# Kernel optimization log

Hardware: AMD Instinct MI355X
Metric: run time of the kernel (lower is better)

Reference implementation:

```python
import jax, jax.numpy as jnp
import numpy as np

B1, B2 = 4096, 4096
DF, MF = 1024, 512
H1, H2, H3, H1_ = 2048, 1024, 512, 1024
DO, MO = 1, 1


def _lin(x, W, b):
    return x @ W.T + b


def setup_inputs() -> dict:
    key = jax.random.key(0)
    ks = jax.random.split(key, 22)

    def w(k, o, i):
        return (jax.random.normal(k, (o, i), jnp.float32) / np.sqrt(i)).astype(jnp.float32)

    def bz(k, o):
        return jax.random.normal(k, (o,), jnp.float32) * 0.01

    return {
        'x1': jax.random.normal(ks[0], (B1, DF), jnp.float32),
        'x2': jax.random.normal(ks[1], (B2, MF), jnp.float32),
        'W1_1': w(ks[2], H1, DF),  'b1_1': bz(ks[3], H1),
        'W1_2': w(ks[4], H2, H1),  'b1_2': bz(ks[5], H2),
        'W1_3': w(ks[6], H3, H2),  'b1_3': bz(ks[7], H3),
        'W1_4': w(ks[8], H2, H3),  'b1_4': bz(ks[9], H2),
        'W1_5': w(ks[10], H1, H2), 'b1_5': bz(ks[11], H1),
        'Wp1':  w(ks[12], DO, H1), 'bp1':  bz(ks[13], DO),
        'W2_1': w(ks[14], H1_, MF), 'b2_1': bz(ks[15], H1_),
        'W2_2': w(ks[16], H3, H1_), 'b2_2': bz(ks[17], H3),
        'W2_3': w(ks[18], H1_, H3), 'b2_3': bz(ks[19], H1_),
        'Wp2':  w(ks[20], MO, H1_), 'bp2':  bz(ks[21], MO),
    }


def reference(x1, x2, W1_1, b1_1, W1_2, b1_2, W1_3, b1_3, W1_4, b1_4,
              W1_5, b1_5, Wp1, bp1, W2_1, b2_1, W2_2, b2_2, W2_3, b2_3,
              Wp2, bp2):
    # dropout: eval mode (identity)
    h = jax.nn.relu(_lin(x1, W1_1, b1_1))
    h = jax.nn.relu(_lin(h, W1_2, b1_2))
    x_1 = jax.nn.sigmoid(_lin(h, W1_3, b1_3))          # [B1, H3]
    h = jax.nn.relu(_lin(x_1, W1_4, b1_4))
    h = jax.nn.relu(_lin(h, W1_5, b1_5))
    x2_1 = jax.nn.sigmoid(_lin(h, Wp1, bp1))           # [B1, DO]

    g = jax.nn.relu(_lin(x2, W2_1, b2_1))
    x_2 = jax.nn.sigmoid(_lin(g, W2_2, b2_2))          # [B2, H3]
    g = jax.nn.relu(_lin(x_2, W2_3, b2_3))
    x2_2 = jax.nn.sigmoid(_lin(g, Wp2, bp2))           # [B2, MO]

    # Python loop over x_1 rows doing (x_2 * row).sum(1) == single GEMM x_1 @ x_2.T
    scores = x_1 @ x_2.T                                # [B1, B2]
    pre_dm = scores.reshape(-1)                         # row-major matches torch.cat order
    # MinMaxScaler.fit_transform on detached values (original uses .data -> no grad)
    pre_dm = jax.lax.stop_gradient(pre_dm)
    mn, mx = pre_dm.min(), pre_dm.max()
    pre_dm = (pre_dm - mn) / (mx - mn)

    pre_data = x2_1.reshape(-1)
    pre_model = x2_2.T.reshape(-1)
    return (pre_data, pre_dm, pre_model)
```

## Files before the change

kernel.cpp:

```cpp
#include <hip/hip_runtime.h>
#include <hip/hip_bf16.h>

typedef __bf16 bf16_t;
typedef bf16_t bf16x8 __attribute__((ext_vector_type(8)));
typedef bf16_t bf16x4 __attribute__((ext_vector_type(4)));
typedef float f32x4 __attribute__((ext_vector_type(4)));

typedef __attribute__((address_space(1))) const void gconst_void;
typedef __attribute__((address_space(3))) void lds_void;

__device__ __forceinline__ void async16(const bf16_t* g, bf16_t* l) {
  __builtin_amdgcn_global_load_lds((gconst_void*)g, (lds_void*)l, 16, 0, 0);
}

struct CvtDesc { const float* src; bf16_t* dst; long n; };
struct CvtArgs { CvtDesc d[10]; };

__global__ __launch_bounds__(256) void cvt_many(CvtArgs a) {
  const CvtDesc de = a.d[blockIdx.y];
  long i = ((long)blockIdx.x * 256 + threadIdx.x) * 4;
  const long stride = (long)gridDim.x * 256 * 4;
  for (; i < de.n; i += stride) {
    float4 v = *(const float4*)(de.src + i);
    bf16x4 o;
    o[0] = (bf16_t)v.x; o[1] = (bf16_t)v.y; o[2] = (bf16_t)v.z; o[3] = (bf16_t)v.w;
    *(bf16x4*)(de.dst + i) = o;
  }
}

struct GDesc {
  const bf16_t* A; const bf16_t* W; const float* bias; void* C;
  int N, K, act;
};
struct GArgs { GDesc d[2]; int ntiles0; };

template <typename OutT, bool MINMAX, int BN>
__global__ __launch_bounds__(256) void gemm_gb(GArgs ga, float* __restrict__ pmin,
                                               float* __restrict__ pmax) {
  constexpr int NJ = BN / 32;
  const int b = blockIdx.x;
  const int p = (b >= ga.ntiles0) ? 1 : 0;
  const GDesc d = ga.d[p];
  const int local = b - (p ? ga.ntiles0 : 0);
  const int bm = (local & 31) * 128;
  const int bn = (local >> 5) * BN;
  const int N = d.N, K = d.K;

  __shared__ __align__(16) bf16_t As[3][128 * 32];
  __shared__ __align__(16) bf16_t Bs[3][BN * 32];

  const int t = threadIdx.x;
  const int wave = t >> 6;
  const int lane = t & 63;
  const int quad = lane >> 4;
  const int l15 = lane & 15;
  const int wm = (wave >> 1) * 64;
  const int wn = (wave & 1) * (BN / 2);

  f32x4 acc[4][NJ];
#pragma unroll
  for (int i = 0; i < 4; ++i)
#pragma unroll
    for (int j = 0; j < NJ; ++j) acc[i][j] = (f32x4){0.f, 0.f, 0.f, 0.f};

  const int c0 = t, c1 = t + 256;
  const int r0 = c0 >> 2, kc0 = ((c0 & 3) - r0 - (r0 >> 2)) & 3;
  const int r1 = c1 >> 2, kc1 = ((c1 & 3) - r1 - (r1 >> 2)) & 3;
  const bf16_t* pa0 = d.A + (long)(bm + r0) * K + kc0 * 8;
  const bf16_t* pa1 = d.A + (long)(bm + r1) * K + kc1 * 8;
  const bf16_t* pw0 = d.W + (long)(bn + r0) * K + kc0 * 8;
  const bf16_t* pw1 = d.W + (long)(bn + r1) * K + kc1 * 8;
  bf16_t* lA0 = &As[0][c0 * 8]; bf16_t* lA1 = &As[0][c1 * 8];
  bf16_t* lB0 = &Bs[0][c0 * 8]; bf16_t* lB1 = &Bs[0][c1 * 8];
  const int bufOffA = 128 * 32;
  const int bufOffB = BN * 32;

  auto stage = [&](int ke, int bi) {
    const int oA = bi * bufOffA, oB = bi * bufOffB;
    async16(pa0 + ke, lA0 + oA);
    async16(pa1 + ke, lA1 + oA);
    async16(pw0 + ke, lB0 + oB);
    if constexpr (BN == 128) async16(pw1 + ke, lB1 + oB);
  };

  auto compute = [&](int bi) {
    const bf16_t* as = As[bi];
    const bf16_t* bs = Bs[bi];
    bf16x8 af[4], bfr[NJ];
#pragma unroll
    for (int i = 0; i < 4; ++i) {
      const int r = wm + i * 16 + l15;
      af[i] = *(const bf16x8*)&as[r * 32 + ((quad + r + (r >> 2)) & 3) * 8];
    }
#pragma unroll
    for (int j = 0; j < NJ; ++j) {
      const int r = wn + j * 16 + l15;
      bfr[j] = *(const bf16x8*)&bs[r * 32 + ((quad + r + (r >> 2)) & 3) * 8];
    }
#pragma unroll
    for (int i = 0; i < 4; ++i)
#pragma unroll
      for (int j = 0; j < NJ; ++j)
        acc[i][j] = __builtin_amdgcn_mfma_f32_16x16x32_bf16(bfr[j], af[i],
                                                            acc[i][j], 0, 0, 0);
  };

  const int nsteps = K >> 5;
  stage(0, 0);
  stage(32, 1);
  int s = 0;
  for (; s < nsteps - 2; ++s) {
    __builtin_amdgcn_s_barrier();
    __builtin_amdgcn_sched_barrier(0);
    stage((s + 2) * 32, (s + 2) % 3);
    if constexpr (BN == 128)
      asm volatile("s_waitcnt vmcnt(8)" ::: "memory");
    else
      asm volatile("s_waitcnt vmcnt(6)" ::: "memory");
    __builtin_amdgcn_s_barrier();
    __builtin_amdgcn_sched_barrier(0);
    compute(s % 3);
  }
  __builtin_amdgcn_s_barrier();
  if constexpr (BN == 128)
    asm volatile("s_waitcnt vmcnt(4)" ::: "memory");
  else
    asm volatile("s_waitcnt vmcnt(3)" ::: "memory");
  __builtin_amdgcn_s_barrier();
  __builtin_amdgcn_sched_barrier(0);
  compute(s % 3);
  ++s;
  asm volatile("s_waitcnt vmcnt(0)" ::: "memory");
  __builtin_amdgcn_s_barrier();
  __builtin_amdgcn_sched_barrier(0);
  compute(s % 3);

  OutT* C = (OutT*)d.C;
  const int row0 = bm + wm + l15;
  const int col0 = bn + wn + quad * 4;
  float mn = 3.4e38f, mx = -3.4e38f;
#pragma unroll
  for (int i = 0; i < 4; ++i) {
    const long row = row0 + i * 16;
#pragma unroll
    for (int j = 0; j < NJ; ++j) {
      const int col = col0 + j * 16;
      f32x4 bv = d.bias ? *(const f32x4*)&d.bias[col] : (f32x4){0.f, 0.f, 0.f, 0.f};
      f32x4 v;
#pragma unroll
      for (int r = 0; r < 4; ++r) {
        float x = acc[i][j][r] + bv[r];
        if (d.act == 1) x = fmaxf(x, 0.f);
        else if (d.act == 2) x = 1.f / (1.f + expf(-x));
        v[r] = x;
        if (MINMAX) { mn = fminf(mn, x); mx = fmaxf(mx, x); }
      }
      if constexpr (sizeof(OutT) == 4) {
        *(f32x4*)&((float*)C)[row * N + col] = v;
      } else {
        bf16x4 o;
        o[0] = (bf16_t)v[0]; o[1] = (bf16_t)v[1];
        o[2] = (bf16_t)v[2]; o[3] = (bf16_t)v[3];
        *(bf16x4*)&((bf16_t*)C)[row * N + col] = o;
      }
    }
  }
  if (MINMAX) {
#pragma unroll
    for (int off = 32; off > 0; off >>= 1) {
      mn = fminf(mn, __shfl_down(mn, off));
      mx = fmaxf(mx, __shfl_down(mx, off));
    }
    __shared__ float smn[4], smx[4];
    if (lane == 0) { smn[wave] = mn; smx[wave] = mx; }
    __syncthreads();
    if (t == 0) {
      pmin[blockIdx.x] = fminf(fminf(smn[0], smn[1]), fminf(smn[2], smn[3]));
      pmax[blockIdx.x] = fmaxf(fmaxf(smx[0], smx[1]), fmaxf(smx[2], smx[3]));
    }
  }
}

struct RDesc { const bf16_t* A; const float* w; const float* b; float* out; int K; };

__global__ __launch_bounds__(64) void rowdot2(RDesc d0, RDesc d1) {
  const RDesc d = blockIdx.y ? d1 : d0;
  const int row = blockIdx.x;
  const int lane = threadIdx.x;
  const bf16_t* a = d.A + (long)row * d.K;
  float s = 0.f;
  for (int k = lane * 8; k < d.K; k += 64 * 8) {
    bf16x8 av = *(const bf16x8*)&a[k];
    float4 w0 = *(const float4*)&d.w[k];
    float4 w1 = *(const float4*)&d.w[k + 4];
    s += (float)av[0] * w0.x + (float)av[1] * w0.y +
         (float)av[2] * w0.z + (float)av[3] * w0.w +
         (float)av[4] * w1.x + (float)av[5] * w1.y +
         (float)av[6] * w1.z + (float)av[7] * w1.w;
  }
#pragma unroll
  for (int off = 32; off > 0; off >>= 1) s += __shfl_down(s, off);
  if (lane == 0) d.out[row] = 1.f / (1.f + expf(-(s + d.b[0])));
}

__global__ __launch_bounds__(256) void minmax_final(
    const float* __restrict__ pmin, const float* __restrict__ pmax, int nb,
    float* __restrict__ res) {
  float mn = 3.4e38f, mx = -3.4e38f;
  for (int i = threadIdx.x; i < nb; i += 256) {
    mn = fminf(mn, pmin[i]);
    mx = fmaxf(mx, pmax[i]);
  }
#pragma unroll
  for (int off = 32; off > 0; off >>= 1) {
    mn = fminf(mn, __shfl_down(mn, off));
    mx = fmaxf(mx, __shfl_down(mx, off));
  }
  __shared__ float smn[4], smx[4];
  const int wv = threadIdx.x >> 6, ln = threadIdx.x & 63;
  if (ln == 0) { smn[wv] = mn; smx[wv] = mx; }
  __syncthreads();
  if (threadIdx.x == 0) {
    float m0 = fminf(fminf(smn[0], smn[1]), fminf(smn[2], smn[3]));
    float m1 = fmaxf(fmaxf(smx[0], smx[1]), fmaxf(smx[2], smx[3]));
    res[0] = m0;
    res[1] = 1.f / (m1 - m0);
  }
}

__global__ __launch_bounds__(256) void normalize_k(
    float* __restrict__ out, const float* __restrict__ res, long n) {
  const float mn = res[0], inv = res[1];
  long i = ((long)blockIdx.x * 256 + threadIdx.x) * 4;
  const long stride = (long)gridDim.x * 256 * 4;
  for (; i < n; i += stride) {
    float4 v = *(const float4*)&out[i];
    v.x = (v.x - mn) * inv;
    v.y = (v.y - mn) * inv;
    v.z = (v.z - mn) * inv;
    v.w = (v.w - mn) * inv;
    *(float4*)&out[i] = v;
  }
}

extern "C" void kernel_launch(void* const* d_in, const int* in_sizes, int n_in,
                              void* d_out, int out_size, void* d_ws,
                              size_t ws_size, hipStream_t stream) {
  const float* x1   = (const float*)d_in[0];
  const float* x2   = (const float*)d_in[1];
  const float* W1_1 = (const float*)d_in[2];   const float* b1_1 = (const float*)d_in[3];
  const float* W1_2 = (const float*)d_in[4];   const float* b1_2 = (const float*)d_in[5];
  const float* W1_3 = (const float*)d_in[6];   const float* b1_3 = (const float*)d_in[7];
  const float* W1_4 = (const float*)d_in[8];   const float* b1_4 = (const float*)d_in[9];
  const float* W1_5 = (const float*)d_in[10];  const float* b1_5 = (const float*)d_in[11];
  const float* Wp1  = (const float*)d_in[12];  const float* bp1  = (const float*)d_in[13];
  const float* W2_1 = (const float*)d_in[14];  const float* b2_1 = (const float*)d_in[15];
  const float* W2_2 = (const float*)d_in[16];  const float* b2_2 = (const float*)d_in[17];
  const float* W2_3 = (const float*)d_in[18];  const float* b2_3 = (const float*)d_in[19];
  const float* Wp2  = (const float*)d_in[20];  const float* bp2  = (const float*)d_in[21];

  float* out = (float*)d_out;
  float* out_pre_data  = out;
  float* out_pre_dm    = out + 4096;
  float* out_pre_model = out + 4096 + (long)4096 * 4096;

  char* arena = (char*)out_pre_dm;
  const size_t MB = 1024 * 1024;
  bf16_t* x1b   = (bf16_t*)(arena);
  bf16_t* x2b   = (bf16_t*)(arena + 8 * MB);
  bf16_t* W1_1b = (bf16_t*)(arena + 12 * MB);
  bf16_t* W1_2b = (bf16_t*)(arena + 16 * MB);
  bf16_t* W1_3b = (bf16_t*)(arena + 20 * MB);
  bf16_t* W1_4b = (bf16_t*)(arena + 21 * MB);
  bf16_t* W1_5b = (bf16_t*)(arena + 22 * MB);
  bf16_t* W2_1b = (bf16_t*)(arena + 26 * MB);
  bf16_t* W2_2b = (bf16_t*)(arena + 27 * MB);
  bf16_t* W2_3b = (bf16_t*)(arena + 28 * MB);
  bf16_t* bufA  = (bf16_t*)(arena + 32 * MB);
  bf16_t* bufB  = (bf16_t*)(arena + 48 * MB);
  bf16_t* bufC  = (bf16_t*)(arena + 56 * MB);

  char* ws = (char*)d_ws;
  bf16_t* bufX1 = (bf16_t*)(ws);
  bf16_t* bufX2 = (bf16_t*)(ws + 4 * MB);
  float* pmin = (float*)(ws + 8 * MB);
  float* pmax = pmin + 2048;
  float* res  = pmax + 2048;

  CvtArgs ca;
  ca.d[0] = {x1,   x1b,   (long)4096 * 1024};
  ca.d[1] = {x2,   x2b,   (long)4096 * 512};
  ca.d[2] = {W1_1, W1_1b, (long)2048 * 1024};
  ca.d[3] = {W1_2, W1_2b, (long)1024 * 2048};
  ca.d[4] = {W1_3, W1_3b, (long)512 * 1024};
  ca.d[5] = {W1_4, W1_4b, (long)1024 * 512};
  ca.d[6] = {W1_5, W1_5b, (long)2048 * 1024};
  ca.d[7] = {W2_1, W2_1b, (long)1024 * 512};
  ca.d[8] = {W2_2, W2_2b, (long)512 * 1024};
  ca.d[9] = {W2_3, W2_3b, (long)1024 * 512};
  cvt_many<<<dim3(192, 10), 256, 0, stream>>>(ca);

  const long nS = (long)4096 * 4096;
  GArgs g;

  g.d[0] = {x1b, W1_1b, b1_1, bufA, 2048, 1024, 1};
  g.d[1] = {x2b, W2_1b, b2_1, bufC, 1024, 512, 1};
  g.ntiles0 = 512;
  gemm_gb<bf16_t, false, 128><<<768, 256, 0, stream>>>(g, nullptr, nullptr);

  g.d[0] = {bufA, W1_2b, b1_2, bufB, 1024, 2048, 1};
  g.d[1] = {bufC, W2_2b, b2_2, bufX2, 512, 1024, 2};
  g.ntiles0 = 512;
  gemm_gb<bf16_t, false, 64><<<768, 256, 0, stream>>>(g, nullptr, nullptr);

  g.d[0] = {bufB, W1_3b, b1_3, bufX1, 512, 1024, 2};
  g.d[1] = {bufX2, W2_3b, b2_3, bufC, 1024, 512, 1};
  g.ntiles0 = 256;
  gemm_gb<bf16_t, false, 64><<<768, 256, 0, stream>>>(g, nullptr, nullptr);

  g.d[0] = {bufX1, W1_4b, b1_4, bufB, 1024, 512, 1};
  g.d[1] = g.d[0];
  g.ntiles0 = 512;
  gemm_gb<bf16_t, false, 64><<<512, 256, 0, stream>>>(g, nullptr, nullptr);

  g.d[0] = {bufB, W1_5b, b1_5, bufA, 2048, 1024, 1};
  g.d[1] = g.d[0];
  g.ntiles0 = 1024;
  gemm_gb<bf16_t, false, 64><<<1024, 256, 0, stream>>>(g, nullptr, nullptr);

  RDesc r0 = {bufA, Wp1, bp1, out_pre_data, 2048};
  RDesc r1 = {bufC, Wp2, bp2, out_pre_model, 1024};
  rowdot2<<<dim3(4096, 2), 64, 0, stream>>>(r0, r1);

  g.d[0] = {bufX1, bufX2, nullptr, out_pre_dm, 4096, 512, 0};
  g.d[1] = g.d[0];
  g.ntiles0 = 1024;
  gemm_gb<float, true, 128><<<1024, 256, 0, stream>>>(g, pmin, pmax);

  minmax_final<<<1, 256, 0, stream>>>(pmin, pmax, 1024, res);
  normalize_k<<<2048, 256, 0, stream>>>(out_pre_dm, res, nS);
}
```

Before: 354.4 us.

## Fuse scores GEMM, min/max reduction and normalization into one cooperative kernel

Replaces the scores GEMM, the min/max final reduction and the normalize pass with a single persistent cooperative kernel. The kernel computes 128x64 tiles with a triple-buffered async LDS pipeline and writes the raw scores. After a grid-wide sync it reduces the per-block min/max and renormalizes the tiles it owns, which are likely still in cache. This removes two kernel launches and targets the separate full pass over the 64MB output. In exchange it adds a grid sync, and it hardcodes 256 compute units when sizing the grid from occupancy.

After: 522.1 us. 1.47x slower.

```diff
diff --git a/kernel.cpp b/kernel.cpp
--- a/kernel.cpp
+++ b/kernel.cpp
@@ -1,5 +1,8 @@
 #include <hip/hip_runtime.h>
 #include <hip/hip_bf16.h>
+#include <hip/hip_cooperative_groups.h>
+
+namespace cg = cooperative_groups;
 
 typedef __bf16 bf16_t;
 typedef bf16_t bf16x8 __attribute__((ext_vector_type(8)));
@@ -181,6 +184,156 @@
   }
 }
 
+__global__ __launch_bounds__(256) void scores_fused(
+    const bf16_t* __restrict__ X1, const bf16_t* __restrict__ X2,
+    float* __restrict__ C, float* __restrict__ pmin, float* __restrict__ pmax) {
+  constexpr int K = 512, N = 4096, NTILES = 2048;
+  __shared__ __align__(16) bf16_t As[3][128 * 32];
+  __shared__ __align__(16) bf16_t Bs[3][64 * 32];
+  __shared__ float smn[4], smx[4];
+
+  const int t = threadIdx.x;
+  const int wave = t >> 6, lane = t & 63, quad = lane >> 4, l15 = lane & 15;
+  const int wm = (wave >> 1) * 64, wn = (wave & 1) * 32;
+  const int c0 = t, c1 = t + 256;
+  const int r0 = c0 >> 2, kc0 = ((c0 & 3) - r0 - (r0 >> 2)) & 3;
+  const int r1 = c1 >> 2, kc1 = ((c1 & 3) - r1 - (r1 >> 2)) & 3;
+  const int bufOffA = 128 * 32, bufOffB = 64 * 32;
+
+  float mn = 3.4e38f, mx = -3.4e38f;
+
+  for (int idx = blockIdx.x; idx < NTILES; idx += gridDim.x) {
+    const int bm = (idx & 31) * 128, bn = (idx >> 5) * 64;
+    const bf16_t* pa0 = X1 + (long)(bm + r0) * K + kc0 * 8;
+    const bf16_t* pa1 = X1 + (long)(bm + r1) * K + kc1 * 8;
+    const bf16_t* pw0 = X2 + (long)(bn + r0) * K + kc0 * 8;
+    bf16_t* lA0 = &As[0][c0 * 8]; bf16_t* lA1 = &As[0][c1 * 8];
+    bf16_t* lB0 = &Bs[0][c0 * 8];
+
+    f32x4 acc[4][2];
+#pragma unroll
+    for (int i = 0; i < 4; ++i)
+#pragma unroll
+      for (int j = 0; j < 2; ++j) acc[i][j] = (f32x4){0.f, 0.f, 0.f, 0.f};
+
+    auto stage = [&](int ke, int bi) {
+      const int oA = bi * bufOffA, oB = bi * bufOffB;
+      async16(pa0 + ke, lA0 + oA);
+      async16(pa1 + ke, lA1 + oA);
+      async16(pw0 + ke, lB0 + oB);
+    };
+    auto compute = [&](int bi) {
+      const bf16_t* as = As[bi];
+      const bf16_t* bs = Bs[bi];
+      bf16x8 af[4], bfr[2];
+#pragma unroll
+      for (int i = 0; i < 4; ++i) {
+        const int r = wm + i * 16 + l15;
+        af[i] = *(const bf16x8*)&as[r * 32 + ((quad + r + (r >> 2)) & 3) * 8];
+      }
+#pragma unroll
+      for (int j = 0; j < 2; ++j) {
+        const int r = wn + j * 16 + l15;
+        bfr[j] = *(const bf16x8*)&bs[r * 32 + ((quad + r + (r >> 2)) & 3) * 8];
+      }
+#pragma unroll
+      for (int i = 0; i < 4; ++i) {
+        acc[i][0] = __builtin_amdgcn_mfma_f32_16x16x32_bf16(bfr[0], af[i],
+                                                            acc[i][0], 0, 0, 0);
+        acc[i][1] = __builtin_amdgcn_mfma_f32_16x16x32_bf16(bfr[1], af[i],
+                                                            acc[i][1], 0, 0, 0);
+      }
+    };
+
+    __syncthreads();
+    stage(0, 0);
+    stage(32, 1);
+    int s = 0;
+    for (; s < 14; ++s) {
+      __builtin_amdgcn_s_barrier();
+      __builtin_amdgcn_sched_barrier(0);
+      stage((s + 2) * 32, (s + 2) % 3);
+      asm volatile("s_waitcnt vmcnt(6)" ::: "memory");
+      __builtin_amdgcn_s_barrier();
+      __builtin_amdgcn_sched_barrier(0);
+      compute(s % 3);
+    }
+    __builtin_amdgcn_s_barrier();
+    asm volatile("s_waitcnt vmcnt(3)" ::: "memory");
+    __builtin_amdgcn_s_barrier();
+    __builtin_amdgcn_sched_barrier(0);
+    compute(14 % 3);
+    asm volatile("s_waitcnt vmcnt(0)" ::: "memory");
+    __builtin_amdgcn_s_barrier();
+    __builtin_amdgcn_sched_barrier(0);
+    compute(15 % 3);
+
+    const int row0 = bm + wm + l15;
+    const int col0 = bn + wn + quad * 4;
+#pragma unroll
+    for (int i = 0; i < 4; ++i) {
+      const long row = row0 + i * 16;
+#pragma unroll
+      for (int j = 0; j < 2; ++j) {
+        const int col = col0 + j * 16;
+        f32x4 v;
+#pragma unroll
+        for (int r = 0; r < 4; ++r) {
+          float x = acc[i][j][r];
+          v[r] = x;
+          mn = fminf(mn, x); mx = fmaxf(mx, x);
+        }
+        *(f32x4*)&C[row * N + col] = v;
+      }
+    }
+  }
+
+#pragma unroll
+  for (int off = 32; off > 0; off >>= 1) {
+    mn = fminf(mn, __shfl_down(mn, off));
+    mx = fmaxf(mx, __shfl_down(mx, off));
+  }
+  if (lane == 0) { smn[wave] = mn; smx[wave] = mx; }
+  __syncthreads();
+  if (t == 0) {
+    pmin[blockIdx.x] = fminf(fminf(smn[0], smn[1]), fminf(smn[2], smn[3]));
+    pmax[blockIdx.x] = fmaxf(fmaxf(smx[0], smx[1]), fmaxf(smx[2], smx[3]));
+  }
+  __threadfence();
+  cg::this_grid().sync();
+
+  float gmn = 3.4e38f, gmx = -3.4e38f;
+  for (int i = t; i < (int)gridDim.x; i += 256) {
+    gmn = fminf(gmn, pmin[i]);
+    gmx = fmaxf(gmx, pmax[i]);
+  }
+#pragma unroll
+  for (int off = 32; off > 0; off >>= 1) {
+    gmn = fminf(gmn, __shfl_down(gmn, off));
+    gmx = fmaxf(gmx, __shfl_down(gmx, off));
+  }
+  __syncthreads();
+  if (lane == 0) { smn[wave] = gmn; smx[wave] = gmx; }
+  __syncthreads();
+  gmn = fminf(fminf(smn[0], smn[1]), fminf(smn[2], smn[3]));
+  gmx = fmaxf(fmaxf(smx[0], smx[1]), fmaxf(smx[2], smx[3]));
+  const float inv = 1.f / (gmx - gmn);
+
+  for (int idx = blockIdx.x; idx < NTILES; idx += gridDim.x) {
+    const int bm = (idx & 31) * 128, bn = (idx >> 5) * 64;
+    const int rr = t >> 4, cc = (t & 15) * 4;
+    for (int r = rr; r < 128; r += 16) {
+      float4* p = (float4*)&C[(long)(bm + r) * N + bn + cc];
+      float4 v = *p;
+      v.x = (v.x - gmn) * inv;
+      v.y = (v.y - gmn) * inv;
+      v.z = (v.z - gmn) * inv;
+      v.w = (v.w - gmn) * inv;
+      *p = v;
+    }
+  }
+}
+
 struct RDesc { const bf16_t* A; const float* w; const float* b; float* out; int K; };
 
 __global__ __launch_bounds__(64) void rowdot2(RDesc d0, RDesc d1) {
@@ -201,46 +354,6 @@
 #pragma unroll
   for (int off = 32; off > 0; off >>= 1) s += __shfl_down(s, off);
   if (lane == 0) d.out[row] = 1.f / (1.f + expf(-(s + d.b[0])));
-}
-
-__global__ __launch_bounds__(256) void minmax_final(
-    const float* __restrict__ pmin, const float* __restrict__ pmax, int nb,
-    float* __restrict__ res) {
-  float mn = 3.4e38f, mx = -3.4e38f;
-  for (int i = threadIdx.x; i < nb; i += 256) {
-    mn = fminf(mn, pmin[i]);
-    mx = fmaxf(mx, pmax[i]);
-  }
-#pragma unroll
-  for (int off = 32; off > 0; off >>= 1) {
-    mn = fminf(mn, __shfl_down(mn, off));
-    mx = fmaxf(mx, __shfl_down(mx, off));
-  }
-  __shared__ float smn[4], smx[4];
-  const int wv = threadIdx.x >> 6, ln = threadIdx.x & 63;
-  if (ln == 0) { smn[wv] = mn; smx[wv] = mx; }
-  __syncthreads();
-  if (threadIdx.x == 0) {
-    float m0 = fminf(fminf(smn[0], smn[1]), fminf(smn[2], smn[3]));
-    float m1 = fmaxf(fmaxf(smx[0], smx[1]), fmaxf(smx[2], smx[3]));
-    res[0] = m0;
-    res[1] = 1.f / (m1 - m0);
-  }
-}
-
-__global__ __launch_bounds__(256) void normalize_k(
-    float* __restrict__ out, const float* __restrict__ res, long n) {
-  const float mn = res[0], inv = res[1];
-  long i = ((long)blockIdx.x * 256 + threadIdx.x) * 4;
-  const long stride = (long)gridDim.x * 256 * 4;
-  for (; i < n; i += stride) {
-    float4 v = *(const float4*)&out[i];
-    v.x = (v.x - mn) * inv;
-    v.y = (v.y - mn) * inv;
-    v.z = (v.z - mn) * inv;
-    v.w = (v.w - mn) * inv;
-    *(float4*)&out[i] = v;
-  }
 }
 
 extern "C" void kernel_launch(void* const* d_in, const int* in_sizes, int n_in,
@@ -285,7 +398,6 @@
   bf16_t* bufX2 = (bf16_t*)(ws + 4 * MB);
   float* pmin = (float*)(ws + 8 * MB);
   float* pmax = pmin + 2048;
-  float* res  = pmax + 2048;
 
   CvtArgs ca;
   ca.d[0] = {x1,   x1b,   (long)4096 * 1024};
@@ -300,7 +412,6 @@
   ca.d[9] = {W2_3, W2_3b, (long)1024 * 512};
   cvt_many<<<dim3(192, 10), 256, 0, stream>>>(ca);
 
-  const long nS = (long)4096 * 4096;
   GArgs g;
 
   g.d[0] = {x1b, W1_1b, b1_1, bufA, 2048, 1024, 1};
@@ -332,11 +443,14 @@
   RDesc r1 = {bufC, Wp2, bp2, out_pre_model, 1024};
   rowdot2<<<dim3(4096, 2), 64, 0, stream>>>(r0, r1);
 
-  g.d[0] = {bufX1, bufX2, nullptr, out_pre_dm, 4096, 512, 0};
-  g.d[1] = g.d[0];
-  g.ntiles0 = 1024;
-  gemm_gb<float, true, 128><<<1024, 256, 0, stream>>>(g, pmin, pmax);
-
-  minmax_final<<<1, 256, 0, stream>>>(pmin, pmax, 1024, res);
-  normalize_k<<<2048, 256, 0, stream>>>(out_pre_dm, res, nS);
-}
+  int nb = 0;
+  hipOccupancyMaxActiveBlocksPerMultiprocessor(&nb, scores_fused, 256, 0);
+  if (nb < 1) nb = 1;
+  int sg = nb * 256;
+  if (sg > 2048) sg = 2048;
+  const bf16_t* sX1 = bufX1;
+  const bf16_t* sX2 = bufX2;
+  float* sC = out_pre_dm;
+  void* kargs[] = {(void*)&sX1, (void*)&sX2, (void*)&sC, (void*)&pmin, (void*)&pmax};
+  hipLaunchCooperativeKernel(scores_fused, dim3(sg), dim3(256), kargs, 0, stream);
+}
```
